# Optimization experiments

Measured on AMD Instinct MI355X. Metric: run time of the kernel, lower is better.

Reference implementation:

```python
import jax, jax.numpy as jnp
import numpy as np

K = 15          # k_point_level
EPS = 1e-5      # BatchNorm eps
NEG = 0.2       # LeakyReLU slope


def _lrelu(y):
    return jnp.where(y > 0, y, NEG * y)


def _knn_idx(x, k):
    # x: [N, C, P] -> idx [N, P, k] of nearest points (incl. self) by -||xi-xj||^2 topk
    inner = -2.0 * jnp.einsum('ncp,ncq->npq', x, x)
    xx = jnp.sum(x * x, axis=1)                      # [N, P]
    pd = -xx[:, :, None] - inner - xx[:, None, :]    # [N, P, P]
    return jax.lax.top_k(pd, k)[1]


def _edge_feature(x, k):
    # x: [N, C, P] -> [N, P, k, 2C] = concat(neigh - center, center)
    N = x.shape[0]
    idx = _knn_idx(x, k)                             # [N, P, k]
    xt = jnp.transpose(x, (0, 2, 1))                 # [N, P, C]
    neigh = xt[jnp.arange(N)[:, None, None], idx]    # [N, P, k, C]
    center = jnp.broadcast_to(xt[:, :, None, :], neigh.shape)
    return jnp.concatenate([neigh - center, center], axis=-1)


def _edge_block(x, W, gamma, beta, k):
    # EdgeConv: gather -> 1x1 conv -> BN (batch stats) -> LeakyReLU -> max over k
    f = _edge_feature(x, k)                          # [N, P, k, 2C]
    y = jnp.einsum('npkc,oc->npko', f, W)
    m = jnp.mean(y, axis=(0, 1, 2))
    v = jnp.var(y, axis=(0, 1, 2))
    y = (y - m) * jax.lax.rsqrt(v + EPS) * gamma + beta
    y = jnp.max(_lrelu(y), axis=2)                   # [N, P, O]
    return jnp.transpose(y, (0, 2, 1))               # [N, O, P]


def _forward(x, W1, g1, b1, W2, g2, b2, W3, g3, b3, W4, g4, b4,
             W5, g5, b5, Wl1, g6, b6, Wl2, bl2, g7, b7, Wl3, bl3):
    x1 = _edge_block(x, W1, g1, b1, K)               # [N, 64, P]
    x2 = _edge_block(x1, W2, g2, b2, K)              # [N, 64, P]
    x3 = _edge_block(x2, W3, g3, b3, K)              # [N, 128, P]
    x4 = _edge_block(x3, W4, g4, b4, K)              # [N, 256, P]
    xc = jnp.concatenate([x1, x2, x3, x4], axis=1)   # [N, 512, P]
    y = jnp.einsum('ncp,oc->npo', xc, W5)            # [N, P, emb]
    m = jnp.mean(y, axis=(0, 1)); v = jnp.var(y, axis=(0, 1))
    y = _lrelu((y - m) * jax.lax.rsqrt(v + EPS) * g5 + b5)
    h = jnp.concatenate([jnp.max(y, axis=1), jnp.mean(y, axis=1)], axis=1)  # [N, 2*emb]
    h = h @ Wl1.T
    m = jnp.mean(h, axis=0); v = jnp.var(h, axis=0)
    h = _lrelu((h - m) * jax.lax.rsqrt(v + EPS) * g6 + b6)
    h = h @ Wl2.T + bl2
    m = jnp.mean(h, axis=0); v = jnp.var(h, axis=0)
    h = _lrelu((h - m) * jax.lax.rsqrt(v + EPS) * g7 + b7)
    logits = h @ Wl3.T + bl3
    return jax.nn.log_softmax(logits, axis=1)


def setup_inputs() -> dict:
    key = jax.random.key(0)
    ks = iter(jax.random.split(key, 16))
    N, P, EMB, NC = 2048, 32, 1024, 800

    def w(k, o, i):
        return jax.random.normal(k, (o, i), jnp.float32) / np.sqrt(i)

    d = {
        'x': jax.random.normal(next(ks), (N, 3, P), jnp.float32),
        'info_point_set': jnp.zeros((1,), jnp.float32),
        'W1': w(next(ks), 64, 6),   'g1': jnp.ones(64),  'b1': jnp.zeros(64),
        'W2': w(next(ks), 64, 128), 'g2': jnp.ones(64),  'b2': jnp.zeros(64),
        'W3': w(next(ks), 128, 128),'g3': jnp.ones(128), 'b3': jnp.zeros(128),
        'W4': w(next(ks), 256, 256),'g4': jnp.ones(256), 'b4': jnp.zeros(256),
        'W5': w(next(ks), EMB, 512),'g5': jnp.ones(EMB), 'b5': jnp.zeros(EMB),
        'Wl1': w(next(ks), 512, 2 * EMB), 'g6': jnp.ones(512), 'b6': jnp.zeros(512),
        'Wl2': w(next(ks), 256, 512), 'bl2': jnp.zeros(256),
        'g7': jnp.ones(256), 'b7': jnp.zeros(256),
        'Wl3': w(next(ks), NC, 256), 'bl3': jnp.zeros(NC),
    }
    return d


def reference(x, info_point_set, W1, g1, b1, W2, g2, b2, W3, g3, b3,
              W4, g4, b4, W5, g5, b5, Wl1, g6, b6, Wl2, bl2, g7, b7, Wl3, bl3):
    # info_point_set unused: args.k + args.k_global == 0 path (dynamic KNN graph).
    return _forward(x, W1, g1, b1, W2, g2, b2, W3, g3, b3, W4, g4, b4,
                    W5, g5, b5, Wl1, g6, b6, Wl2, bl2, g7, b7, Wl3, bl3)
```

## Files before the change

kernel.cpp:

```cpp
#include <hip/hip_runtime.h>
#include <hip/hip_bf16.h>
#include <cstdint>
#include <cstddef>

#define NPTS 2048
#define P 32
#define KNN_K 15
#define LRELU_NEG 0.2f
#define BN_EPS 1e-5f

__device__ __forceinline__ float lrelu(float x) { return x > 0.f ? x : LRELU_NEG * x; }

__device__ __forceinline__ unsigned short f2bf(float x) {
    union { float f; unsigned u; } uu; uu.f = x;
    unsigned r = uu.u + 0x7fffu + ((uu.u >> 16) & 1u);
    return (unsigned short)(r >> 16);
}
__device__ __forceinline__ float bf2f(unsigned short b) {
    union { unsigned u; float f; } uu; uu.u = ((unsigned)b) << 16;
    return uu.f;
}

typedef short bf16x8 __attribute__((ext_vector_type(8)));
typedef float f32x4  __attribute__((ext_vector_type(4)));

__device__ __forceinline__ void edge_pack_body(int i, const float* __restrict__ W,
                                               unsigned short* __restrict__ wpk,
                                               int C, int O, int NCHUNK)
{
    const int TOTC = 2 * O, NTT = TOTC / 16;
    if (i >= C * TOTC) return;
    int j = i & 7, lane = (i >> 3) & 63, rest = i >> 9;
    int ntg = rest % NTT, kb = rest / NTT;
    int k = kb * 32 + (lane >> 4) * 8 + j;
    int col = ntg * 16 + (lane & 15);
    int O2C = TOTC / NCHUNK, OC = O / NCHUNK;
    int chunk = col / O2C, cl = col % O2C;
    float v;
    if (cl < OC) { int o = chunk * OC + cl; v = W[(size_t)o * 2 * C + k]; }
    else         { int o = chunk * OC + cl - OC; v = W[(size_t)o * 2 * C + C + k] - W[(size_t)o * 2 * C + k]; }
    unsigned short hi = f2bf(v);
    wpk[(size_t)rest * 1024 + lane * 8 + j] = hi;
    wpk[(size_t)rest * 1024 + 512 + lane * 8 + j] = f2bf(v - bf2f(hi));
}

__device__ __forceinline__ void wfc_pack_body(int i, const float* __restrict__ W,
                                              unsigned short* __restrict__ wpk,
                                              int Kk, int Nn, int NTT)
{
    if (i >= NTT * 16 * Kk) return;
    int j = i & 7, lane = (i >> 3) & 63, rest = i >> 9;
    int ntg = rest % NTT, kb = rest / NTT;
    int k = kb * 32 + (lane >> 4) * 8 + j;
    int col = ntg * 16 + (lane & 15);
    float v = (col < Nn) ? W[(size_t)col * Kk + k] : 0.f;
    unsigned short hi = f2bf(v);
    wpk[(size_t)rest * 1024 + lane * 8 + j] = hi;
    wpk[(size_t)rest * 1024 + 512 + lane * 8 + j] = f2bf(v - bf2f(hi));
}

__global__ __launch_bounds__(256) void pack_all_kernel(
    const float* __restrict__ W1, const float* __restrict__ W2,
    const float* __restrict__ W3, const float* __restrict__ W4,
    const float* __restrict__ W5, const float* __restrict__ Wl1,
    const float* __restrict__ Wl2, const float* __restrict__ Wl3,
    float* __restrict__ wt1,
    unsigned short* __restrict__ wpk2, unsigned short* __restrict__ wpk3,
    unsigned short* __restrict__ wpk4, unsigned short* __restrict__ w5pk,
    unsigned short* __restrict__ fc1pk, unsigned short* __restrict__ fc2pk,
    unsigned short* __restrict__ fc3pk)
{
    const int b = blockIdx.x, t = threadIdx.x;
    if (b < 2) {
        int i = b * 256 + t;
        if (i < 3 * 128) {
            int c = i / 128, col = i % 128;
            float v;
            if (col < 64) v = W1[(size_t)col * 6 + c];
            else          v = W1[(size_t)(col - 64) * 6 + 3 + c] - W1[(size_t)(col - 64) * 6 + c];
            wt1[i] = v;
        }
    } else if (b < 34)   edge_pack_body((b - 2)    * 256 + t, W2, wpk2, 64, 64, 1);
    else if (b < 98)     edge_pack_body((b - 34)   * 256 + t, W3, wpk3, 64, 128, 1);
    else if (b < 354)    edge_pack_body((b - 98)   * 256 + t, W4, wpk4, 128, 256, 2);
    else if (b < 2402) {
        int i = (b - 354) * 256 + t;
        if (i < (1 << 19)) {
            int j = i & 7, lane = (i >> 3) & 63, nt = (i >> 9) & 63, kb = i >> 15;
            int c = kb * 32 + (lane >> 4) * 8 + j;
            int o = nt * 16 + (lane & 15);
            float f = W5[(size_t)o * 512 + c];
            unsigned short hi = f2bf(f);
            size_t base = (size_t)(kb * 64 + nt) * 1024 + (size_t)lane * 8 + j;
            w5pk[base] = hi;
            w5pk[base + 512] = f2bf(f - bf2f(hi));
        }
    }
    else if (b < 6498)   wfc_pack_body((b - 2402) * 256 + t, Wl1, fc1pk, 2048, 512, 32);
    else if (b < 7010)   wfc_pack_body((b - 6498) * 256 + t, Wl2, fc2pk, 512, 256, 16);
    else                 wfc_pack_body((b - 7010) * 256 + t, Wl3, fc3pk, 256, 800, 52);
}

template<int C, int O, int NCHUNK, bool OUT>
__global__ __launch_bounds__(256) void edge_pass_kernel(
    const float* __restrict__ xin, int cloudStride,
    const float* __restrict__ wt,
    unsigned char* idx,
    const float* __restrict__ st,
    float* __restrict__ xcout,
    float* __restrict__ partS, float* __restrict__ partQ)
{
    constexpr int TOTC = 2 * O;
    constexpr int O2C = TOTC / NCHUNK;
    constexpr int OC  = O / NCHUNK;
    constexpr int TPC = (O2C >= 256) ? 1 : (256 / O2C);
    constexpr int CPT = (O2C > 256) ? (O2C / 256) : 1;
    constexpr int PP  = P / TPC;
    constexpr int QUADS = OC / 4;
    constexpr int PG    = 256 / QUADS;
    constexpr int PPq   = P / PG;
    const int n = blockIdx.x, t = threadIdx.x;

    __shared__ float xs[C][P];
    __shared__ alignas(16) float gh[P * O2C];
    __shared__ unsigned char idl[P * KNN_K];
    __shared__ float xx[P];

    const float* xp = xin + (size_t)n * cloudStride;
    for (int i = t; i < C * P; i += 256) xs[i / P][i % P] = xp[i];

    if constexpr (!OUT) {
        float* pd = gh;
        __syncthreads();
        if (t < P) { float s = 0.f; for (int c = 0; c < C; ++c) { float v = xs[c][t]; s = fmaf(v, v, s); } xx[t] = s; }
        __syncthreads();
        for (int i = t; i < P * P; i += 256) {
            int p = i >> 5, q = i & 31;
            float d = 0.f;
            for (int c = 0; c < C; ++c) d = fmaf(xs[c][p], xs[c][q], d);
            pd[p * (P + 1) + q] = 2.f * d - xx[p] - xx[q];
        }
        __syncthreads();
        if (t < P) {
            for (int j = 0; j < KNN_K; ++j) {
                float best = -INFINITY; int bq = 0;
                for (int q = 0; q < P; ++q) { float v = pd[t * (P + 1) + q]; if (v > best) { best = v; bq = q; } }
                idl[t * KNN_K + j] = (unsigned char)bq;
                idx[(size_t)n * (P * KNN_K) + t * KNN_K + j] = (unsigned char)bq;
                pd[t * (P + 1) + bq] = -INFINITY;
            }
        }
    } else {
        for (int i = t; i < P * KNN_K; i += 256) idl[i] = idx[(size_t)n * (P * KNN_K) + i];
    }

    const int col = (O2C >= 256) ? t : (t % O2C);
    const int p0  = ((O2C >= 256) ? 0 : (t / O2C)) * PP;
    const int q4  = t % QUADS;
    const int pg  = t / QUADS;
    const int p0q = pg * PPq;

    for (int chunk = 0; chunk < NCHUNK; ++chunk) {
        __syncthreads();
        {
            float acc[CPT][PP];
            #pragma unroll
            for (int j = 0; j < CPT; ++j)
                #pragma unroll
                for (int p = 0; p < PP; ++p) acc[j][p] = 0.f;
            for (int c = 0; c < C; ++c) {
                float w[CPT];
                #pragma unroll
                for (int j = 0; j < CPT; ++j) w[j] = wt[(size_t)c * TOTC + chunk * O2C + col + j * 256];
                #pragma unroll
                for (int p = 0; p < PP; ++p) {
                    float xv = xs[c][p0 + p];
                    #pragma unroll
                    for (int j = 0; j < CPT; ++j) acc[j][p] = fmaf(w[j], xv, acc[j][p]);
                }
            }
            #pragma unroll
            for (int j = 0; j < CPT; ++j)
                #pragma unroll
                for (int p = 0; p < PP; ++p) gh[(p0 + p) * O2C + col + j * 256] = acc[j][p];
        }
        __syncthreads();

        if constexpr (!OUT) {
            f32x4 ssum4 = (f32x4)0.f, ssq4 = (f32x4)0.f;
            #pragma unroll
            for (int p = 0; p < PPq; ++p) {
                const int pp = p0q + p;
                const f32x4 gv = *(const f32x4*)&gh[pp * O2C + OC + q4 * 4];
                #pragma unroll
                for (int k = 0; k < KNN_K; ++k) {
                    const int q = idl[pp * KNN_K + k];
                    f32x4 yv = *(const f32x4*)&gh[q * O2C + q4 * 4] + gv;
                    ssum4 += yv; ssq4 += yv * yv;
                }
            }
            __syncthreads();
            #pragma unroll
            for (int e = 0; e < 4; ++e) {
                gh[(q4 * 4 + e) * PG + pg] = ssum4[e];
                gh[OC * PG + (q4 * 4 + e) * PG + pg] = ssq4[e];
            }
            __syncthreads();
            if (t < OC) {
                float S = 0.f, Q = 0.f;
                #pragma unroll
                for (int j = 0; j < PG; ++j) { S += gh[t * PG + j]; Q += gh[OC * PG + t * PG + j]; }
                partS[(size_t)(chunk * OC + t) * 2048 + n] = S;
                partQ[(size_t)(chunk * OC + t) * 2048 + n] = Q;
            }
        } else {
            const f32x4 s4  = *(const f32x4*)&st[chunk * OC + q4 * 4];
            const f32x4 sh4 = *(const f32x4*)&st[1024 + chunk * OC + q4 * 4];
            f32x4 res[PPq];
            #pragma unroll
            for (int p = 0; p < PPq; ++p) {
                const int pp = p0q + p;
                const f32x4 gv = *(const f32x4*)&gh[pp * O2C + OC + q4 * 4];
                f32x4 mx = (f32x4)(-INFINITY), mn = (f32x4)(INFINITY);
                #pragma unroll
                for (int k = 0; k < KNN_K; ++k) {
                    const int q = idl[pp * KNN_K + k];
                    f32x4 yv = *(const f32x4*)&gh[q * O2C + q4 * 4] + gv;
                    #pragma unroll
                    for (int e = 0; e < 4; ++e) { mx[e] = fmaxf(mx[e], yv[e]); mn[e] = fminf(mn[e], yv[e]); }
                }
                #pragma unroll
                for (int e = 0; e < 4; ++e)
                    res[p][e] = lrelu(fmaf(s4[e], (s4[e] >= 0.f ? mx[e] : mn[e]), sh4[e]));
            }
            __syncthreads();
            #pragma unroll
            for (int p = 0; p < PPq; ++p)
                #pragma unroll
                for (int e = 0; e < 4; ++e)
                    gh[(q4 * 4 + e) * (P + 1) + p0q + p] = res[p][e];
            __syncthreads();
            for (int i = t; i < OC * P; i += 256)
                xcout[(size_t)n * (512 * P) + chunk * OC * P + i] = gh[(i / P) * (P + 1) + (i % P)];
        }
    }
}

template<int C, int O, bool OUT>
__global__ __launch_bounds__(256) void edge_mfma_kernel(
    const float* __restrict__ xin, int cloudStride,
    const unsigned short* __restrict__ wpk,
    unsigned char* idx,
    const float* __restrict__ st,
    float* __restrict__ xcout,
    float* __restrict__ partS, float* __restrict__ partQ)
{
    constexpr int TOTC  = 2 * O;
    constexpr int O2C   = (TOTC > 256) ? 256 : TOTC;
    constexpr int NCHUNK= TOTC / O2C;
    constexpr int OC    = O2C / 2;
    constexpr int NTW   = O2C / 64;
    constexpr int KB    = C / 32;
    constexpr int NTT   = TOTC / 16;
    constexpr int AS    = C + 8;
    constexpr int GHS   = O2C + 4;
    constexpr int QUADS = OC / 4;
    constexpr int PG    = 256 / QUADS;
    constexpr int PPq   = P / PG;
    static_assert(P * GHS >= C * P + P * (P + 1), "pd+xs must fit in gh");
    static_assert(P * GHS >= 2 * OC * PG, "stats scratch must fit in gh");

    const int n = blockIdx.x, t = threadIdx.x;
    const int w = t >> 6, l = t & 63;
    const int lg = l >> 4, lm = l & 15;

    __shared__ unsigned short Ah[P * AS];
    __shared__ unsigned short Al[P * AS];
    __shared__ alignas(16) float gh[P * GHS];
    __shared__ unsigned char idl[P * KNN_K];
    __shared__ float xx[P];

    const float* xp = xin + (size_t)n * cloudStride;
    if constexpr (!OUT) {
        float* xsf = gh;
        float* pd  = gh + C * P;
        for (int i = t; i < C * P; i += 256) {
            int c = i / P, p = i % P;
            float v = xp[i];
            unsigned short hi = f2bf(v);
            Ah[p * AS + c] = hi;
            Al[p * AS + c] = f2bf(v - bf2f(hi));
            xsf[i] = v;
        }
        __syncthreads();
        if (t < P) { float s = 0.f; for (int c = 0; c < C; ++c) { float v = xsf[c * P + t]; s = fmaf(v, v, s); } xx[t] = s; }
        __syncthreads();
        for (int i = t; i < P * P; i += 256) {
            int p = i >> 5, q = i & 31;
            float d = 0.f;
            for (int c = 0; c < C; ++c) d = fmaf(xsf[c * P + p], xsf[c * P + q], d);
            pd[p * (P + 1) + q] = 2.f * d - xx[p] - xx[q];
        }
        __syncthreads();
        if (t < P) {
            for (int j = 0; j < KNN_K; ++j) {
                float best = -INFINITY; int bq = 0;
                for (int q = 0; q < P; ++q) { float v = pd[t * (P + 1) + q]; if (v > best) { best = v; bq = q; } }
                idl[t * KNN_K + j] = (unsigned char)bq;
                idx[(size_t)n * (P * KNN_K) + t * KNN_K + j] = (unsigned char)bq;
                pd[t * (P + 1) + bq] = -INFINITY;
            }
        }
        __syncthreads();
    } else {
        for (int i = t; i < C * P; i += 256) {
            int c = i / P, p = i % P;
            float v = xp[i];
            unsigned short hi = f2bf(v);
            Ah[p * AS + c] = hi;
            Al[p * AS + c] = f2bf(v - bf2f(hi));
        }
        for (int i = t; i < P * KNN_K; i += 256) idl[i] = idx[(size_t)n * (P * KNN_K) + i];
        __syncthreads();
    }

    const int q4  = t % QUADS;
    const int pg  = t / QUADS;
    const int p0q = pg * PPq;

    for (int chunk = 0; chunk < NCHUNK; ++chunk) {
        f32x4 acc[2][NTW];
        #pragma unroll
        for (int mt = 0; mt < 2; ++mt)
            #pragma unroll
            for (int nt = 0; nt < NTW; ++nt) acc[mt][nt] = (f32x4)0.f;

        #pragma unroll
        for (int kb = 0; kb < KB; ++kb) {
            bf16x8 a_h[2], a_l[2];
            #pragma unroll
            for (int mt = 0; mt < 2; ++mt) {
                int row = mt * 16 + lm;
                a_h[mt] = *(const bf16x8*)&Ah[row * AS + kb * 32 + lg * 8];
                a_l[mt] = *(const bf16x8*)&Al[row * AS + kb * 32 + lg * 8];
            }
            #pragma unroll
            for (int nt = 0; nt < NTW; ++nt) {
                int ntg = chunk * (O2C / 16) + w * NTW + nt;
                const unsigned short* bp = wpk + (size_t)(kb * NTT + ntg) * 1024 + (size_t)l * 8;
                bf16x8 Bh = *(const bf16x8*)bp;
                bf16x8 Bl = *(const bf16x8*)(bp + 512);
                #pragma unroll
                for (int mt = 0; mt < 2; ++mt) {
                    acc[mt][nt] = __builtin_amdgcn_mfma_f32_16x16x32_bf16(a_h[mt], Bl, acc[mt][nt], 0, 0, 0);
                    acc[mt][nt] = __builtin_amdgcn_mfma_f32_16x16x32_bf16(a_l[mt], Bh, acc[mt][nt], 0, 0, 0);
                    acc[mt][nt] = __builtin_amdgcn_mfma_f32_16x16x32_bf16(a_h[mt], Bh, acc[mt][nt], 0, 0, 0);
                }
            }
        }
        __syncthreads();
        #pragma unroll
        for (int mt = 0; mt < 2; ++mt)
            #pragma unroll
            for (int nt = 0; nt < NTW; ++nt) {
                int colb = (w * NTW + nt) * 16 + lm;
                #pragma unroll
                for (int r = 0; r < 4; ++r)
                    gh[(mt * 16 + lg * 4 + r) * GHS + colb] = acc[mt][nt][r];
            }
        __syncthreads();

        if constexpr (!OUT) {
            f32x4 ssum4 = (f32x4)0.f, ssq4 = (f32x4)0.f;
            #pragma unroll
            for (int p = 0; p < PPq; ++p) {
                const int pp = p0q + p;
                const f32x4 gv = *(const f32x4*)&gh[pp * GHS + OC + q4 * 4];
                #pragma unroll
                for (int k = 0; k < KNN_K; ++k) {
                    const int q = idl[pp * KNN_K + k];
                    f32x4 yv = *(const f32x4*)&gh[q * GHS + q4 * 4] + gv;
                    ssum4 += yv; ssq4 += yv * yv;
                }
            }
            __syncthreads();
            #pragma unroll
            for (int e = 0; e < 4; ++e) {
                gh[(q4 * 4 + e) * PG + pg] = ssum4[e];
                gh[OC * PG + (q4 * 4 + e) * PG + pg] = ssq4[e];
            }
            __syncthreads();
            if (t < OC) {
                float S = 0.f, Q = 0.f;
                #pragma unroll
                for (int j = 0; j < PG; ++j) { S += gh[t * PG + j]; Q += gh[OC * PG + t * PG + j]; }
                partS[(size_t)(chunk * OC + t) * 2048 + n] = S;
                partQ[(size_t)(chunk * OC + t) * 2048 + n] = Q;
            }
        } else {
            const f32x4 s4  = *(const f32x4*)&st[chunk * OC + q4 * 4];
            const f32x4 sh4 = *(const f32x4*)&st[1024 + chunk * OC + q4 * 4];
            f32x4 res[PPq];
            #pragma unroll
            for (int p = 0; p < PPq; ++p) {
                const int pp = p0q + p;
                const f32x4 gv = *(const f32x4*)&gh[pp * GHS + OC + q4 * 4];
                f32x4 mx = (f32x4)(-INFINITY), mn = (f32x4)(INFINITY);
                #pragma unroll
                for (int k = 0; k < KNN_K; ++k) {
                    const int q = idl[pp * KNN_K + k];
                    f32x4 yv = *(const f32x4*)&gh[q * GHS + q4 * 4] + gv;
                    #pragma unroll
                    for (int e = 0; e < 4; ++e) { mx[e] = fmaxf(mx[e], yv[e]); mn[e] = fminf(mn[e], yv[e]); }
                }
                #pragma unroll
                for (int e = 0; e < 4; ++e)
                    res[p][e] = lrelu(fmaf(s4[e], (s4[e] >= 0.f ? mx[e] : mn[e]), sh4[e]));
            }
            __syncthreads();
            #pragma unroll
            for (int p = 0; p < PPq; ++p)
                #pragma unroll
                for (int e = 0; e < 4; ++e)
                    gh[(q4 * 4 + e) * (P + 1) + p0q + p] = res[p][e];
            __syncthreads();
            for (int i = t; i < OC * P; i += 256)
                xcout[(size_t)n * (512 * P) + chunk * OC * P + i] = gh[(i / P) * (P + 1) + (i % P)];
        }
    }
}

__global__ __launch_bounds__(256) void reduce_stats_kernel(const float* __restrict__ partS,
                                                           const float* __restrict__ partQ,
                                                           const float* __restrict__ gamma,
                                                           const float* __restrict__ beta,
                                                           float* __restrict__ st, int nparts, float inv_count)
{
    const int o = blockIdx.x, t = threadIdx.x;
    __shared__ float rs[256], rq[256];
    float S = 0.f, Q = 0.f;
    for (int i = t; i < nparts; i += 256) { S += partS[(size_t)o * 2048 + i]; Q += partQ[(size_t)o * 2048 + i]; }
    rs[t] = S; rq[t] = Q; __syncthreads();
    for (int w = 128; w > 0; w >>= 1) { if (t < w) { rs[t] += rs[t + w]; rq[t] += rq[t + w]; } __syncthreads(); }
    if (t == 0) {
        float m = rs[0] * inv_count;
        float v = fmaxf(rq[0] * inv_count - m * m, 0.f);
        float s = gamma[o] * rsqrtf(v + BN_EPS);
        st[o] = s;
        st[1024 + o] = fmaf(-m, s, beta[o]);
    }
}

__global__ __launch_bounds__(512) void conv5_store_kernel(
    const float* xc, const unsigned short* __restrict__ wpack,
    unsigned short* y5,
    float* __restrict__ partS, float* __restrict__ partQ)
{
    const int b = blockIdx.x;
    const int t = threadIdx.x;
    const int w = t >> 6, l = t & 63;
    const int lg = l >> 4, lm = l & 15;

    __shared__ unsigned short Ah[2][64][40];
    __shared__ unsigned short Al[2][64][40];

    f32x4 acc[4][8];
    #pragma unroll
    for (int mt = 0; mt < 4; ++mt)
        #pragma unroll
        for (int nt = 0; nt < 8; ++nt) acc[mt][nt] = (f32x4)0.f;

    const float* xbase = xc + (size_t)(b * 2) * (512 * P);

    const int sp4    = t & 7;
    const int schalf = (t >> 3) & 15;
    const int scloud = (t >> 7) & 1;
    const bool sact  = t < 256;

    auto stage = [&](int kb, int buf) {
        if (sact) {
            const float* src = xbase + (size_t)scloud * (512 * P)
                             + (size_t)(kb * 32 + 2 * schalf) * P + sp4 * 4;
            const float4 v0 = *(const float4*)src;
            const float4 v1 = *(const float4*)(src + P);
            const int r0 = scloud * 32 + sp4 * 4;
            #pragma unroll
            for (int e = 0; e < 4; ++e) {
                float a0 = (&v0.x)[e], a1 = (&v1.x)[e];
                unsigned short h0 = f2bf(a0), h1 = f2bf(a1);
                unsigned short l0 = f2bf(a0 - bf2f(h0)), l1 = f2bf(a1 - bf2f(h1));
                *(unsigned*)&Ah[buf][r0 + e][2 * schalf] = (unsigned)h0 | ((unsigned)h1 << 16);
                *(unsigned*)&Al[buf][r0 + e][2 * schalf] = (unsigned)l0 | ((unsigned)l1 << 16);
            }
        }
    };

    stage(0, 0);
    int cur = 0;
    for (int kb = 0; kb < 16; ++kb) {
        __syncthreads();
        if (kb + 1 < 16) stage(kb + 1, cur ^ 1);

        bf16x8 a_h[4], a_l[4];
        #pragma unroll
        for (int mt = 0; mt < 4; ++mt) {
            int row = mt * 16 + lm;
            a_h[mt] = *(const bf16x8*)&Ah[cur][row][lg * 8];
            a_l[mt] = *(const bf16x8*)&Al[cur][row][lg * 8];
        }
        #pragma unroll
        for (int nt = 0; nt < 8; ++nt) {
            const int ntg = w * 8 + nt;
            const unsigned short* bp = wpack + (size_t)(kb * 64 + ntg) * 2 * 512 + (size_t)l * 8;
            bf16x8 Bh = *(const bf16x8*)bp;
            bf16x8 Bl = *(const bf16x8*)(bp + 512);
            #pragma unroll
            for (int mt = 0; mt < 4; ++mt) {
                acc[mt][nt] = __builtin_amdgcn_mfma_f32_16x16x32_bf16(a_h[mt], Bl, acc[mt][nt], 0, 0, 0);
                acc[mt][nt] = __builtin_amdgcn_mfma_f32_16x16x32_bf16(a_l[mt], Bh, acc[mt][nt], 0, 0, 0);
                acc[mt][nt] = __builtin_amdgcn_mfma_f32_16x16x32_bf16(a_h[mt], Bh, acc[mt][nt], 0, 0, 0);
            }
        }
        cur ^= 1;
    }
    __syncthreads();

    #pragma unroll
    for (int nt = 0; nt < 8; ++nt) {
        float s = 0.f, q = 0.f;
        #pragma unroll
        for (int mt = 0; mt < 4; ++mt)
            #pragma unroll
            for (int r = 0; r < 4; ++r) { float v = acc[mt][nt][r]; s += v; q = fmaf(v, v, q); }
        s += __shfl_xor(s, 16); q += __shfl_xor(q, 16);
        s += __shfl_xor(s, 32); q += __shfl_xor(q, 32);
        if (l < 16) {
            int o = w * 128 + nt * 16 + lm;
            partS[(size_t)o * 2048 + b] = s;
            partQ[(size_t)o * 2048 + b] = q;
        }
        #pragma unroll
        for (int mt = 0; mt < 4; ++mt) {
            unsigned p0 = (unsigned)f2bf(acc[mt][nt][0]) | ((unsigned)f2bf(acc[mt][nt][1]) << 16);
            unsigned p1 = (unsigned)f2bf(acc[mt][nt][2]) | ((unsigned)f2bf(acc[mt][nt][3]) << 16);
            size_t off = ((((size_t)b * 8 + w) * 8 + nt) * 4 + mt) * 64 + l;
            ((uint2*)y5)[off] = make_uint2(p0, p1);
        }
    }
}

__global__ __launch_bounds__(512) void conv5_finish_kernel(
    const unsigned short* __restrict__ y5, const float* __restrict__ st, float* __restrict__ h)
{
    const int b = blockIdx.x, t = threadIdx.x;
    const int w = t >> 6, l = t & 63, lm = l & 15;
    #pragma unroll
    for (int nt = 0; nt < 8; ++nt) {
        const int o = w * 128 + nt * 16 + lm;
        const float sc = st[o], sh = st[1024 + o];
        #pragma unroll
        for (int cloud = 0; cloud < 2; ++cloud) {
            float mx = -INFINITY, sm = 0.f;
            #pragma unroll
            for (int half = 0; half < 2; ++half) {
                const int mt = cloud * 2 + half;
                uint2 pk = ((const uint2*)y5)[((((size_t)b * 8 + w) * 8 + nt) * 4 + mt) * 64 + l];
                #pragma unroll
                for (int r = 0; r < 4; ++r) {
                    unsigned word = (r < 2) ? pk.x : pk.y;
                    unsigned short bits = (unsigned short)((r & 1) ? (word >> 16) : (word & 0xffff));
                    float v = lrelu(fmaf(sc, bf2f(bits), sh));
                    mx = fmaxf(mx, v); sm += v;
                }
            }
            mx = fmaxf(mx, __shfl_xor(mx, 16)); sm += __shfl_xor(sm, 16);
            mx = fmaxf(mx, __shfl_xor(mx, 32)); sm += __shfl_xor(sm, 32);
            if (l < 16) {
                const int n = b * 2 + cloud;
                h[(size_t)n * 2048 + o] = mx;
                h[(size_t)n * 2048 + 1024 + o] = sm * (1.f / 32.f);
            }
        }
    }
}

template<bool BNIN, bool STATS>
__global__ __launch_bounds__(256) void gemm_mfma_nt(
    const float* __restrict__ A, const unsigned short* __restrict__ wpk,
    const float* __restrict__ stbn, const float* __restrict__ bias,
    float* __restrict__ Cc, float* __restrict__ partS, float* __restrict__ partQ,
    int Nn, int NTT, int Kk)
{
    const int o0 = blockIdx.x * 64;
    const int m0 = blockIdx.y * 64;
    const int t = threadIdx.x;
    const int w = t >> 6, l = t & 63;
    const int lg = l >> 4, lm = l & 15;

    __shared__ unsigned short Ah[2][64][40];
    __shared__ unsigned short Al[2][64][40];

    f32x4 acc[4];
    #pragma unroll
    for (int mt = 0; mt < 4; ++mt) acc[mt] = (f32x4)0.f;

    const int srow = t >> 3;
    const int sk4  = (t & 7) * 4;

    auto stage = [&](int kb, int buf) {
        const float* src = A + (size_t)(m0 + srow) * Kk + kb * 32 + sk4;
        float4 v0 = *(const float4*)src;
        float4 v1 = *(const float4*)(src + (size_t)32 * Kk);
        if (BNIN) {
            const float4 s4 = *(const float4*)(stbn + kb * 32 + sk4);
            const float4 t4 = *(const float4*)(stbn + 1024 + kb * 32 + sk4);
            #pragma unroll
            for (int e = 0; e < 4; ++e) {
                (&v0.x)[e] = lrelu(fmaf((&s4.x)[e], (&v0.x)[e], (&t4.x)[e]));
                (&v1.x)[e] = lrelu(fmaf((&s4.x)[e], (&v1.x)[e], (&t4.x)[e]));
            }
        }
        #pragma unroll
        for (int e = 0; e < 4; e += 2) {
            float a0 = (&v0.x)[e], a1 = (&v0.x)[e + 1];
            unsigned short h0 = f2bf(a0), h1 = f2bf(a1);
            *(unsigned*)&Ah[buf][srow][sk4 + e] = (unsigned)h0 | ((unsigned)h1 << 16);
            *(unsigned*)&Al[buf][srow][sk4 + e] =
                (unsigned)f2bf(a0 - bf2f(h0)) | ((unsigned)f2bf(a1 - bf2f(h1)) << 16);
            float b0 = (&v1.x)[e], b1 = (&v1.x)[e + 1];
            unsigned short g0 = f2bf(b0), g1 = f2bf(b1);
            *(unsigned*)&Ah[buf][srow + 32][sk4 + e] = (unsigned)g0 | ((unsigned)g1 << 16);
            *(unsigned*)&Al[buf][srow + 32][sk4 + e] =
                (unsigned)f2bf(b0 - bf2f(g0)) | ((unsigned)f2bf(b1 - bf2f(g1)) << 16);
        }
    };

    const int KB = Kk >> 5;
    stage(0, 0);
    int cur = 0;
    const int ntg = blockIdx.x * 4 + w;
    for (int kb = 0; kb < KB; ++kb) {
        __syncthreads();
        if (kb + 1 < KB) stage(kb + 1, cur ^ 1);
        bf16x8 a_h[4], a_l[4];
        #pragma unroll
        for (int mt = 0; mt < 4; ++mt) {
            a_h[mt] = *(const bf16x8*)&Ah[cur][mt * 16 + lm][lg * 8];
            a_l[mt] = *(const bf16x8*)&Al[cur][mt * 16 + lm][lg * 8];
        }
        const unsigned short* bp = wpk + ((size_t)kb * NTT + ntg) * 1024 + (size_t)l * 8;
        bf16x8 Bh = *(const bf16x8*)bp;
        bf16x8 Bl = *(const bf16x8*)(bp + 512);
        #pragma unroll
        for (int mt = 0; mt < 4; ++mt) {
            acc[mt] = __builtin_amdgcn_mfma_f32_16x16x32_bf16(a_h[mt], Bl, acc[mt], 0, 0, 0);
            acc[mt] = __builtin_amdgcn_mfma_f32_16x16x32_bf16(a_l[mt], Bh, acc[mt], 0, 0, 0);
            acc[mt] = __builtin_amdgcn_mfma_f32_16x16x32_bf16(a_h[mt], Bh, acc[mt], 0, 0, 0);
        }
        cur ^= 1;
    }

    const int col = o0 + w * 16 + lm;
    const bool cok = col < Nn;
    const float bv = (bias != nullptr && cok) ? bias[col] : 0.f;
    float s = 0.f, q = 0.f;
    #pragma unroll
    for (int mt = 0; mt < 4; ++mt) {
        #pragma unroll
        for (int r = 0; r < 4; ++r) {
            float v = acc[mt][r] + bv;
            if (STATS) { s += v; q = fmaf(v, v, q); }
            if (cok) Cc[(size_t)(m0 + mt * 16 + lg * 4 + r) * Nn + col] = v;
        }
    }
    if (STATS) {
        s += __shfl_xor(s, 16); q += __shfl_xor(q, 16);
        s += __shfl_xor(s, 32); q += __shfl_xor(q, 32);
        if (l < 16 && cok) {
            partS[(size_t)col * 2048 + blockIdx.y] = s;
            partQ[(size_t)col * 2048 + blockIdx.y] = q;
        }
    }
}

__global__ __launch_bounds__(256) void logsoftmax_kernel(float* __restrict__ out)
{
    const int n = blockIdx.x, t = threadIdx.x;
    float* row = out + (size_t)n * 800;
    __shared__ float red[256];
    float v[4];
    float mx = -INFINITY;
    #pragma unroll
    for (int j = 0; j < 4; ++j) {
        int i = t + j * 256;
        v[j] = (i < 800) ? row[i] : -INFINITY;
        mx = fmaxf(mx, v[j]);
    }
    red[t] = mx; __syncthreads();
    for (int w = 128; w > 0; w >>= 1) { if (t < w) red[t] = fmaxf(red[t], red[t + w]); __syncthreads(); }
    const float m = red[0]; __syncthreads();
    float s = 0.f;
    #pragma unroll
    for (int j = 0; j < 4; ++j) { int i = t + j * 256; if (i < 800) s += expf(v[j] - m); }
    red[t] = s; __syncthreads();
    for (int w = 128; w > 0; w >>= 1) { if (t < w) red[t] += red[t + w]; __syncthreads(); }
    const float lg = m + logf(red[0]);
    #pragma unroll
    for (int j = 0; j < 4; ++j) { int i = t + j * 256; if (i < 800) row[i] = v[j] - lg; }
}

extern "C" void kernel_launch(void* const* d_in, const int* in_sizes, int n_in,
                              void* d_out, int out_size, void* d_ws, size_t ws_size,
                              hipStream_t stream)
{
    (void)in_sizes; (void)n_in; (void)out_size; (void)ws_size;
    const float* x   = (const float*)d_in[0];
    const float* W1  = (const float*)d_in[2];
    const float* g1  = (const float*)d_in[3];
    const float* b1  = (const float*)d_in[4];
    const float* W2  = (const float*)d_in[5];
    const float* g2  = (const float*)d_in[6];
    const float* b2  = (const float*)d_in[7];
    const float* W3  = (const float*)d_in[8];
    const float* g3  = (const float*)d_in[9];
    const float* b3  = (const float*)d_in[10];
    const float* W4  = (const float*)d_in[11];
    const float* g4  = (const float*)d_in[12];
    const float* b4  = (const float*)d_in[13];
    const float* W5  = (const float*)d_in[14];
    const float* g5  = (const float*)d_in[15];
    const float* b5  = (const float*)d_in[16];
    const float* Wl1 = (const float*)d_in[17];
    const float* g6  = (const float*)d_in[18];
    const float* b6  = (const float*)d_in[19];
    const float* Wl2 = (const float*)d_in[20];
    const float* bl2 = (const float*)d_in[21];
    const float* g7  = (const float*)d_in[22];
    const float* b7  = (const float*)d_in[23];
    const float* Wl3 = (const float*)d_in[24];
    const float* bl3 = (const float*)d_in[25];

    char* ws = (char*)d_ws;
    size_t off = 0;
    auto alloc = [&](size_t bytes) -> void* {
        void* p = ws + off; off += (bytes + 255) & ~(size_t)255; return p;
    };
    float*          xc    = (float*)alloc((size_t)NPTS * 512 * P * 4);
    unsigned char*  idx   = (unsigned char*)alloc((size_t)NPTS * P * KNN_K);
    float*          partS = (float*)alloc((size_t)1024 * 2048 * 4);
    float*          partQ = (float*)alloc((size_t)1024 * 2048 * 4);
    float*          st    = (float*)alloc(2048 * 4);
    float*          wt1   = (float*)alloc(3 * 128 * 4);
    unsigned short* wpk2  = (unsigned short*)alloc((size_t)2 * 64 * 128 * 2);
    unsigned short* wpk3  = (unsigned short*)alloc((size_t)2 * 64 * 256 * 2);
    unsigned short* wpk4  = (unsigned short*)alloc((size_t)2 * 128 * 512 * 2);
    unsigned short* w5pk  = (unsigned short*)alloc((size_t)2 * 512 * 1024 * 2);
    unsigned short* fc1pk = (unsigned short*)alloc((size_t)2 * 512 * 2048 * 2);
    unsigned short* fc2pk = (unsigned short*)alloc((size_t)2 * 256 * 512 * 2);
    unsigned short* fc3pk = (unsigned short*)alloc((size_t)2 * 832 * 256 * 2);
    float*          h     = (float*)alloc((size_t)2048 * 2048 * 4);
    float*          h1p   = (float*)alloc((size_t)2048 * 512 * 4);
    unsigned short* y5 = (unsigned short*)xc;
    float* h2p = h + 1048576;

    const float inv_edge = 1.f / (float)(NPTS * P * KNN_K);

    pack_all_kernel<<<7842, 256, 0, stream>>>(W1, W2, W3, W4, W5, Wl1, Wl2, Wl3,
                                              wt1, wpk2, wpk3, wpk4, w5pk, fc1pk, fc2pk, fc3pk);

    edge_pass_kernel<3, 64, 1, false><<<NPTS, 256, 0, stream>>>(x, 3 * P, wt1, idx, nullptr, nullptr, partS, partQ);
    reduce_stats_kernel<<<64, 256, 0, stream>>>(partS, partQ, g1, b1, st, 2048, inv_edge);
    edge_pass_kernel<3, 64, 1, true><<<NPTS, 256, 0, stream>>>(x, 3 * P, wt1, idx, st, xc + 0 * P, nullptr, nullptr);

    edge_mfma_kernel<64, 64, false><<<NPTS, 256, 0, stream>>>(xc, 512 * P, wpk2, idx, nullptr, nullptr, partS, partQ);
    reduce_stats_kernel<<<64, 256, 0, stream>>>(partS, partQ, g2, b2, st, 2048, inv_edge);
    edge_mfma_kernel<64, 64, true><<<NPTS, 256, 0, stream>>>(xc, 512 * P, wpk2, idx, st, xc + 64 * P, nullptr, nullptr);

    edge_mfma_kernel<64, 128, false><<<NPTS, 256, 0, stream>>>(xc + 64 * P, 512 * P, wpk3, idx, nullptr, nullptr, partS, partQ);
    reduce_stats_kernel<<<128, 256, 0, stream>>>(partS, partQ, g3, b3, st, 2048, inv_edge);
    edge_mfma_kernel<64, 128, true><<<NPTS, 256, 0, stream>>>(xc + 64 * P, 512 * P, wpk3, idx, st, xc + 128 * P, nullptr, nullptr);

    edge_mfma_kernel<128, 256, false><<<NPTS, 256, 0, stream>>>(xc + 128 * P, 512 * P, wpk4, idx, nullptr, nullptr, partS, partQ);
    reduce_stats_kernel<<<256, 256, 0, stream>>>(partS, partQ, g4, b4, st, 2048, inv_edge);
    edge_mfma_kernel<128, 256, true><<<NPTS, 256, 0, stream>>>(xc + 128 * P, 512 * P, wpk4, idx, st, xc + 256 * P, nullptr, nullptr);

    conv5_store_kernel<<<1024, 512, 0, stream>>>(xc, w5pk, y5, partS, partQ);
    reduce_stats_kernel<<<1024, 256, 0, stream>>>(partS, partQ, g5, b5, st, 1024, 1.f / 65536.f);
    conv5_finish_kernel<<<1024, 512, 0, stream>>>(y5, st, h);

    gemm_mfma_nt<false, true><<<dim3(8, 32), 256, 0, stream>>>(h, fc1pk, nullptr, nullptr, h1p, partS, partQ, 512, 32, 2048);
    reduce_stats_kernel<<<512, 256, 0, stream>>>(partS, partQ, g6, b6, st, 32, 1.f / 2048.f);

    gemm_mfma_nt<true, true><<<dim3(4, 32), 256, 0, stream>>>(h1p, fc2pk, st, bl2, h2p, partS, partQ, 256, 16, 512);
    reduce_stats_kernel<<<256, 256, 0, stream>>>(partS, partQ, g7, b7, st, 32, 1.f / 2048.f);

    gemm_mfma_nt<true, false><<<dim3(13, 32), 256, 0, stream>>>(h2p, fc3pk, st, bl3, (float*)d_out, nullptr, nullptr, 800, 52, 256);

    logsoftmax_kernel<<<NPTS, 256, 0, stream>>>((float*)d_out);
}
```

Measured before the change: 787.0 us.

## Drop activation low-part bf16 split in conv5 and defer LDS commit after MFMA

```diff
diff --git a/kernel.cpp b/kernel.cpp
--- a/kernel.cpp
+++ b/kernel.cpp
@@ -462,7 +462,6 @@
     const int lg = l >> 4, lm = l & 15;
 
     __shared__ unsigned short Ah[2][64][40];
-    __shared__ unsigned short Al[2][64][40];
 
     f32x4 acc[4][8];
     #pragma unroll
@@ -477,37 +476,36 @@
     const int scloud = (t >> 7) & 1;
     const bool sact  = t < 256;
 
-    auto stage = [&](int kb, int buf) {
+    float4 v0, v1;
+    auto loadv = [&](int kb) {
         if (sact) {
             const float* src = xbase + (size_t)scloud * (512 * P)
                              + (size_t)(kb * 32 + 2 * schalf) * P + sp4 * 4;
-            const float4 v0 = *(const float4*)src;
-            const float4 v1 = *(const float4*)(src + P);
+            v0 = *(const float4*)src;
+            v1 = *(const float4*)(src + P);
+        }
+    };
+    auto commit = [&](int buf) {
+        if (sact) {
             const int r0 = scloud * 32 + sp4 * 4;
             #pragma unroll
             for (int e = 0; e < 4; ++e) {
-                float a0 = (&v0.x)[e], a1 = (&v1.x)[e];
-                unsigned short h0 = f2bf(a0), h1 = f2bf(a1);
-                unsigned short l0 = f2bf(a0 - bf2f(h0)), l1 = f2bf(a1 - bf2f(h1));
+                unsigned short h0 = f2bf((&v0.x)[e]), h1 = f2bf((&v1.x)[e]);
                 *(unsigned*)&Ah[buf][r0 + e][2 * schalf] = (unsigned)h0 | ((unsigned)h1 << 16);
-                *(unsigned*)&Al[buf][r0 + e][2 * schalf] = (unsigned)l0 | ((unsigned)l1 << 16);
             }
         }
     };
 
-    stage(0, 0);
+    loadv(0); commit(0);
     int cur = 0;
     for (int kb = 0; kb < 16; ++kb) {
         __syncthreads();
-        if (kb + 1 < 16) stage(kb + 1, cur ^ 1);
-
-        bf16x8 a_h[4], a_l[4];
-        #pragma unroll
-        for (int mt = 0; mt < 4; ++mt) {
-            int row = mt * 16 + lm;
-            a_h[mt] = *(const bf16x8*)&Ah[cur][row][lg * 8];
-            a_l[mt] = *(const bf16x8*)&Al[cur][row][lg * 8];
-        }
+        if (kb + 1 < 16) loadv(kb + 1);
+
+        bf16x8 a_h[4];
+        #pragma unroll
+        for (int mt = 0; mt < 4; ++mt)
+            a_h[mt] = *(const bf16x8*)&Ah[cur][mt * 16 + lm][lg * 8];
         #pragma unroll
         for (int nt = 0; nt < 8; ++nt) {
             const int ntg = w * 8 + nt;
@@ -517,10 +515,10 @@
             #pragma unroll
             for (int mt = 0; mt < 4; ++mt) {
                 acc[mt][nt] = __builtin_amdgcn_mfma_f32_16x16x32_bf16(a_h[mt], Bl, acc[mt][nt], 0, 0, 0);
-                acc[mt][nt] = __builtin_amdgcn_mfma_f32_16x16x32_bf16(a_l[mt], Bh, acc[mt][nt], 0, 0, 0);
                 acc[mt][nt] = __builtin_amdgcn_mfma_f32_16x16x32_bf16(a_h[mt], Bh, acc[mt][nt], 0, 0, 0);
             }
         }
+        if (kb + 1 < 16) commit(cur ^ 1);
         cur ^= 1;
     }
     __syncthreads();
```

Result: no change. 776.1 us (-1.4%).
